# Kernel tuning notes

Measured on AMD Instinct MI355X. Metric: run time of the kernel, lower is better.

## Reference

```python
import jax, jax.numpy as jnp
import numpy as np

N = 100000      # num_nodes
E = 1600000     # num_edges (avg degree 16)
D_IN = 128
D_H = 128
D_OUT = 128


def _init_linear(key, out_dim, in_dim):
    # Kaiming-uniform-like init, bound = 1/sqrt(fan_in)
    bound = 1.0 / np.sqrt(in_dim)
    return jax.random.uniform(key, (out_dim, in_dim), jnp.float32, -bound, bound)


def setup_inputs() -> dict:
    key = jax.random.key(0)
    ks = jax.random.split(key, 12)
    x = jax.random.normal(ks[0], (N, D_IN), jnp.float32)
    edge_index = jax.random.randint(ks[1], (2, E), 0, N, jnp.int32)
    dims = [(D_H, D_IN), (D_H, D_H), (D_OUT, D_H)]
    inp = {"x": x, "edge_index": edge_index}
    for i, (do, di) in enumerate(dims):
        inp[f"Wl{i}"] = _init_linear(ks[2 + 3 * i], do, di)      # lin_l: applied to aggregated neighbors
        inp[f"bl{i}"] = jnp.zeros((do,), jnp.float32)
        inp[f"Wr{i}"] = _init_linear(ks[3 + 3 * i], do, di)      # lin_r: applied to root (self) features
    return inp


def _sage_conv(x, src, dst, Wl, bl, Wr):
    # mean aggregation of source-node features at destination nodes
    msg = x[src]                                                   # [E, d]
    agg = jax.ops.segment_sum(msg, dst, num_segments=N)            # [N, d]
    deg = jax.ops.segment_sum(jnp.ones((src.shape[0],), x.dtype), dst, num_segments=N)
    mean = agg / jnp.maximum(deg, 1.0)[:, None]
    return mean @ Wl.T + bl + x @ Wr.T


def reference(x, edge_index, Wl0, bl0, Wr0, Wl1, bl1, Wr1, Wl2, bl2, Wr2):
    src, dst = edge_index[0], edge_index[1]
    # dropout is identity in eval mode
    h = jax.nn.relu(_sage_conv(x, src, dst, Wl0, bl0, Wr0))
    h = jax.nn.relu(_sage_conv(h, src, dst, Wl1, bl1, Wr1))
    return _sage_conv(h, src, dst, Wl2, bl2, Wr2)
```

## Files before the change

kernel.cpp:

```cpp
#include <hip/hip_runtime.h>
#include <hip/hip_bf16.h>

typedef __attribute__((ext_vector_type(8))) short bf16x8;
typedef __attribute__((ext_vector_type(4))) float f32x4;

#define D 128
#define P2CAP 8192


__global__ __launch_bounds__(256) void k_setup(
    const float* __restrict__ x,
    const float* __restrict__ w0, const float* __restrict__ w1,
    const float* __restrict__ w2, const float* __restrict__ w3,
    const float* __restrict__ w4, const float* __restrict__ w5,
    __hip_bfloat16* __restrict__ xb, __hip_bfloat16* __restrict__ wb,
    int* __restrict__ bhist, int xpair)
{
    int t = blockIdx.x * 256 + threadIdx.x;
    if (t < 512) bhist[t] = 0;
    if (t < xpair) {
        float2 f = ((const float2*)x)[t];
        ((__hip_bfloat162*)xb)[t] = __float22bfloat162_rn(f);
    }
    if (t < 6 * 8192) {
        int wsel = t >> 13, wi = t & 8191;
        const float* wp = w0;
        if (wsel == 1) wp = w1;
        else if (wsel == 2) wp = w2;
        else if (wsel == 3) wp = w3;
        else if (wsel == 4) wp = w4;
        else if (wsel == 5) wp = w5;
        float2 f = ((const float2*)wp)[wi];
        ((__hip_bfloat162*)wb)[t] = __float22bfloat162_rn(f);
    }
}


__global__ __launch_bounds__(256) void k_p0(const int* __restrict__ dst,
                                            int* __restrict__ bhist, int e, int n, int epb) {
    __shared__ int lh[512];
    for (int i = threadIdx.x; i < 512; i += 256) lh[i] = 0;
    __syncthreads();
    int lo = blockIdx.x * epb;
    int hi = lo + epb; if (hi > e) hi = e;
    for (int i = lo + threadIdx.x; i < hi; i += 256) {
        int d = dst[i]; d = ((unsigned)d < (unsigned)n) ? d : 0;
        atomicAdd(&lh[d >> 8], 1);
    }
    __syncthreads();
    for (int i = threadIdx.x; i < 512; i += 256)
        if (lh[i]) atomicAdd(&bhist[i], lh[i]);
}

__global__ void k_bscan(const int* __restrict__ bhist, int* __restrict__ bbase,
                        int* __restrict__ bcursor, int nb) {
    __shared__ int lds[512];
    int t = threadIdx.x;
    int v = (t < nb) ? bhist[t] : 0;
    lds[t] = v;
    __syncthreads();
    for (int off = 1; off < 512; off <<= 1) {
        int x = (t >= off) ? lds[t - off] : 0;
        __syncthreads();
        lds[t] += x;
        __syncthreads();
    }
    if (t < nb) { int b = lds[t] - v; bbase[t] = b; bcursor[t] = b; }
    if (t == nb) bbase[t] = lds[nb - 1];
}

__global__ __launch_bounds__(256) void k_p1(const int* __restrict__ src,
                                            const int* __restrict__ dst,
                                            int* __restrict__ bcursor,
                                            int* __restrict__ tmp, int e, int n, int epb) {
    __shared__ int lh[512], gb[512];
    for (int i = threadIdx.x; i < 512; i += 256) lh[i] = 0;
    __syncthreads();
    int lo = blockIdx.x * epb;
    int hi = lo + epb; if (hi > e) hi = e;
    for (int i = lo + threadIdx.x; i < hi; i += 256) {
        int d = dst[i]; d = ((unsigned)d < (unsigned)n) ? d : 0;
        atomicAdd(&lh[d >> 8], 1);
    }
    __syncthreads();
    for (int i = threadIdx.x; i < 512; i += 256) {
        int c = lh[i];
        gb[i] = c ? atomicAdd(&bcursor[i], c) : 0;
    }
    __syncthreads();
    for (int i = threadIdx.x; i < 512; i += 256) lh[i] = 0;
    __syncthreads();
    for (int i = lo + threadIdx.x; i < hi; i += 256) {
        int d = dst[i]; d = ((unsigned)d < (unsigned)n) ? d : 0;
        int s = src[i]; s = ((unsigned)s < (unsigned)n) ? s : 0;
        int b = d >> 8;
        int p = gb[b] + atomicAdd(&lh[b], 1);
        tmp[p] = s | ((d & 255) << 17);
    }
}

__global__ __launch_bounds__(256) void k_p2(const int* __restrict__ tmp,
                                            const int* __restrict__ bbase,
                                            int* __restrict__ deg, int* __restrict__ offs,
                                            int* __restrict__ csr, int n) {
    __shared__ int hist[256], loc[256], cur[256];
    __shared__ int out[P2CAP];
    int b = blockIdx.x, t = threadIdx.x;
    int base = bbase[b];
    int cnt = bbase[b + 1] - base;
    int nodes = n - b * 256; if (nodes > 256) nodes = 256;
    hist[t] = 0;
    __syncthreads();
    for (int i = t; i < cnt; i += 256)
        atomicAdd(&hist[(tmp[base + i] >> 17) & 255], 1);
    __syncthreads();
    int v = hist[t];
    loc[t] = v;
    __syncthreads();
    for (int off = 1; off < 256; off <<= 1) {
        int x = (t >= off) ? loc[t - off] : 0;
        __syncthreads();
        loc[t] += x;
        __syncthreads();
    }
    int myloc = loc[t] - v;
    cur[t] = myloc;
    if (t < nodes) { deg[b * 256 + t] = v; offs[b * 256 + t] = base + myloc; }
    __syncthreads();
    if (cnt <= P2CAP) {
        for (int i = t; i < cnt; i += 256) {
            int e = tmp[base + i];
            int p = atomicAdd(&cur[(e >> 17) & 255], 1);
            out[p] = e & 0x1FFFF;
        }
        __syncthreads();
        for (int i = t; i < cnt; i += 256) csr[base + i] = out[i];
    } else {
        for (int i = t; i < cnt; i += 256) {
            int e = tmp[base + i];
            int p = atomicAdd(&cur[(e >> 17) & 255], 1);
            csr[base + p] = e & 0x1FFFF;
        }
    }
}


__device__ __forceinline__ void acc_int4(float* acc, int4 d) {
    acc[0] += __uint_as_float((unsigned)d.x << 16);
    acc[1] += __uint_as_float((unsigned)d.x & 0xffff0000u);
    acc[2] += __uint_as_float((unsigned)d.y << 16);
    acc[3] += __uint_as_float((unsigned)d.y & 0xffff0000u);
    acc[4] += __uint_as_float((unsigned)d.z << 16);
    acc[5] += __uint_as_float((unsigned)d.z & 0xffff0000u);
    acc[6] += __uint_as_float((unsigned)d.w << 16);
    acc[7] += __uint_as_float((unsigned)d.w & 0xffff0000u);
}

__global__ __launch_bounds__(256) void k_agg(
    const __hip_bfloat16* __restrict__ h,
    const int* __restrict__ csr,
    const int* __restrict__ offs,
    const int* __restrict__ deg,
    __hip_bfloat16* __restrict__ mean,
    int n)
{
    int node = blockIdx.x * 4 + (threadIdx.x >> 6);
    int lane = threadIdx.x & 63;
    if (node >= n) return;
    int grp = lane >> 4;
    int sub = lane & 15;
    int start = offs[node];
    int cnt = deg[node];

    float acc[8];
    #pragma unroll
    for (int k = 0; k < 8; ++k) acc[k] = 0.f;

    const char* hb = (const char*)h;
    int i = 0;
    int bulk = cnt & ~15;

    for (; i < bulk; i += 16) {
        int4 d[4];
        #pragma unroll
        for (int u = 0; u < 4; ++u) {
            int s = csr[start + i + u * 4 + grp];
            s = ((unsigned)s < (unsigned)n) ? s : 0;
            d[u] = *(const int4*)(hb + (size_t)s * 256 + sub * 16);
        }
        #pragma unroll
        for (int u = 0; u < 4; ++u) acc_int4(acc, d[u]);
    }

    if (i < cnt) {
        int4 d[4];
        #pragma unroll
        for (int u = 0; u < 4; ++u) {
            int e = i + u * 4 + grp;
            int ec = (e < cnt) ? e : (cnt - 1);
            int s = csr[start + ec];
            s = ((unsigned)s < (unsigned)n) ? s : 0;
            d[u] = *(const int4*)(hb + (size_t)s * 256 + sub * 16);
            if (e >= cnt) { d[u].x = 0; d[u].y = 0; d[u].z = 0; d[u].w = 0; }
        }
        #pragma unroll
        for (int u = 0; u < 4; ++u) acc_int4(acc, d[u]);
    }

    #pragma unroll
    for (int k = 0; k < 8; ++k) {
        acc[k] += __shfl_xor(acc[k], 16);
        acc[k] += __shfl_xor(acc[k], 32);
    }

    if (grp == 0) {
        float inv = 1.0f / fmaxf((float)cnt, 1.0f);
        union { int4 i4; __hip_bfloat162 h2[4]; } u;
        #pragma unroll
        for (int k = 0; k < 4; ++k)
            u.h2[k] = __float22bfloat162_rn(make_float2(acc[2 * k] * inv, acc[2 * k + 1] * inv));
        *(int4*)((char*)mean + (size_t)node * 256 + sub * 16) = u.i4;
    }
}


__global__ __launch_bounds__(256) void k_gemm(
    const __hip_bfloat16* __restrict__ A0,
    const __hip_bfloat16* __restrict__ A1,
    const __hip_bfloat16* __restrict__ Wb,
    const float* __restrict__ bias,
    float* __restrict__ outF,
    __hip_bfloat16* __restrict__ outB,
    int n, int do_relu)
{
    __shared__ __hip_bfloat16 lW[2 * 128 * 128];

    for (int g = threadIdx.x; g < 4096; g += 256) {
        int half = g >> 11;
        int rem  = g & 2047;
        int row  = rem >> 4;
        int c    = rem & 15;
        bf16x8 v = *(const bf16x8*)(Wb + half * 16384 + row * 128 + c * 8);
        *(bf16x8*)(lW + half * 16384 + row * 128 + ((c ^ (row & 7)) * 8)) = v;
    }
    __syncthreads();

    int w = threadIdx.x >> 6;
    int lane = threadIdx.x & 63;
    int m = lane & 15;
    int q = lane >> 4;
    int base = blockIdx.x * 256 + w * 64;

    f32x4 acc[4][8];
    #pragma unroll
    for (int r = 0; r < 4; ++r)
        #pragma unroll
        for (int i = 0; i < 8; ++i) acc[r][i] = (f32x4){0.f, 0.f, 0.f, 0.f};

    const __hip_bfloat16* Aps[2] = {A0, A1};

    #pragma unroll
    for (int half = 0; half < 2; ++half) {
        const __hip_bfloat16* A = Aps[half];
        #pragma unroll
        for (int kk = 0; kk < 4; ++kk) {
            bf16x8 af[4];
            #pragma unroll
            for (int r = 0; r < 4; ++r) {
                int arow = base + r * 16 + m;
                if (arow > n - 1) arow = n - 1;
                af[r] = *(const bf16x8*)(A + (size_t)arow * D + kk * 32 + q * 8);
            }
            #pragma unroll
            for (int nt = 0; nt < 8; ++nt) {
                int row = nt * 16 + m;
                int c = (kk * 4 + q) ^ (m & 7);
                bf16x8 bf = *(const bf16x8*)(lW + half * 16384 + row * 128 + c * 8);
                #pragma unroll
                for (int r = 0; r < 4; ++r)
                    acc[r][nt] = __builtin_amdgcn_mfma_f32_16x16x32_bf16(af[r], bf, acc[r][nt], 0, 0, 0);
            }
        }
    }

    #pragma unroll
    for (int r = 0; r < 4; ++r) {
        #pragma unroll
        for (int nt = 0; nt < 8; ++nt) {
            int col = nt * 16 + m;
            float b = bias[col];
            #pragma unroll
            for (int rr = 0; rr < 4; ++rr) {
                int row = base + r * 16 + q * 4 + rr;
                if (row < n) {
                    float v = acc[r][nt][rr] + b;
                    if (do_relu) v = fmaxf(v, 0.f);
                    if (outF) outF[(size_t)row * D + col] = v;
                    else      outB[(size_t)row * D + col] = __float2bfloat16(v);
                }
            }
        }
    }
}


extern "C" void kernel_launch(void* const* d_in, const int* in_sizes, int n_in,
                              void* d_out, int out_size, void* d_ws, size_t ws_size,
                              hipStream_t stream) {
    const float* x   = (const float*)d_in[0];
    const int*   ei  = (const int*)d_in[1];
    const float* Wl0 = (const float*)d_in[2];
    const float* bl0 = (const float*)d_in[3];
    const float* Wr0 = (const float*)d_in[4];
    const float* Wl1 = (const float*)d_in[5];
    const float* bl1 = (const float*)d_in[6];
    const float* Wr1 = (const float*)d_in[7];
    const float* Wl2 = (const float*)d_in[8];
    const float* bl2 = (const float*)d_in[9];
    const float* Wr2 = (const float*)d_in[10];

    const int n = in_sizes[0] / D;
    const int e = in_sizes[1] / 2;
    const int* src = ei;
    const int* dst = ei + e;
    const int nb = (n + 255) >> 8;

    uintptr_t p = ((uintptr_t)d_ws + 255) & ~(uintptr_t)255;
    auto carve = [&](size_t bytes) {
        uintptr_t r = p;
        p = (p + bytes + 255) & ~(uintptr_t)255;
        return (void*)r;
    };
    int* deg     = (int*)carve((size_t)n * 4);
    int* offs    = (int*)carve((size_t)n * 4);
    int* bhist   = (int*)carve(512 * 4);
    int* bbase   = (int*)carve(513 * 4);
    int* bcursor = (int*)carve(512 * 4);
    int* csr     = (int*)carve((size_t)e * 4);
    __hip_bfloat16* mean = (__hip_bfloat16*)carve((size_t)n * D * 2);
    __hip_bfloat16* F1   = (__hip_bfloat16*)carve((size_t)n * D * 2);
    __hip_bfloat16* Wb   = (__hip_bfloat16*)carve((size_t)6 * D * D * 2);
    (void)ws_size; (void)n_in; (void)out_size;

    __hip_bfloat16* h0 = (__hip_bfloat16*)d_out;
    int* tmp = (int*)((char*)d_out + (size_t)n * D * 2);

    const int xpair = n * D / 2;

    k_setup<<<(xpair + 255) / 256, 256, 0, stream>>>(
        x, Wl0, Wr0, Wl1, Wr1, Wl2, Wr2, F1, Wb, bhist, xpair);

    const int epb0 = (e + 511) / 512;
    k_p0<<<512, 256, 0, stream>>>(dst, bhist, e, n, epb0);
    k_bscan<<<1, 512, 0, stream>>>(bhist, bbase, bcursor, nb);
    const int epb1 = 8192;
    k_p1<<<(e + epb1 - 1) / epb1, 256, 0, stream>>>(src, dst, bcursor, tmp, e, n, epb1);
    k_p2<<<nb, 256, 0, stream>>>(tmp, bbase, deg, offs, csr, n);

    const int ag = (n + 3) / 4;
    const int gg = (n + 255) / 256;

    __hip_bfloat16* Wb0 = Wb + 0 * 2 * D * D;
    __hip_bfloat16* Wb1 = Wb + 1 * 2 * D * D;
    __hip_bfloat16* Wb2 = Wb + 2 * 2 * D * D;

    k_agg<<<ag, 256, 0, stream>>>(F1, csr, offs, deg, mean, n);
    k_gemm<<<gg, 256, 0, stream>>>(mean, F1, Wb0, bl0, nullptr, h0, n, 1);
    k_agg<<<ag, 256, 0, stream>>>(h0, csr, offs, deg, mean, n);
    k_gemm<<<gg, 256, 0, stream>>>(mean, h0, Wb1, bl1, nullptr, F1, n, 1);
    k_agg<<<ag, 256, 0, stream>>>(F1, csr, offs, deg, mean, n);
    k_gemm<<<gg, 256, 0, stream>>>(mean, F1, Wb2, bl2, (float*)d_out, nullptr, n, 0);
}
```

Measured before the change: 437.9 us.

## Fuse histogram into setup, pack aggregation math, widen GEMM blocks

Merges the destination-bucket histogram pass into the setup conversion kernel and zeroes the histogram with a memset, which removes one launch. The aggregation kernel now accumulates in packed float2 vectors, drops the index bounds clamp and uses 32-bit address arithmetic to cut ALU work. The GEMM runs 512 threads per block, each wave holding 32 rows instead of 64, which lowers register pressure and adds waves. The scatter pass also uses smaller edge chunks. Removing the clamp means an out-of-range index would now read out of bounds.

```diff
diff --git a/kernel.cpp b/kernel.cpp
--- a/kernel.cpp
+++ b/kernel.cpp
@@ -3,6 +3,7 @@
 
 typedef __attribute__((ext_vector_type(8))) short bf16x8;
 typedef __attribute__((ext_vector_type(4))) float f32x4;
+typedef __attribute__((ext_vector_type(2))) float f32x2;
 
 #define D 128
 #define P2CAP 8192
@@ -14,10 +15,10 @@
     const float* __restrict__ w2, const float* __restrict__ w3,
     const float* __restrict__ w4, const float* __restrict__ w5,
     __hip_bfloat16* __restrict__ xb, __hip_bfloat16* __restrict__ wb,
-    int* __restrict__ bhist, int xpair)
+    int* __restrict__ bhist, const int* __restrict__ dst,
+    int xpair, int e, int n, int epb)
 {
     int t = blockIdx.x * 256 + threadIdx.x;
-    if (t < 512) bhist[t] = 0;
     if (t < xpair) {
         float2 f = ((const float2*)x)[t];
         ((__hip_bfloat162*)xb)[t] = __float22bfloat162_rn(f);
@@ -33,24 +34,22 @@
         float2 f = ((const float2*)wp)[wi];
         ((__hip_bfloat162*)wb)[t] = __float22bfloat162_rn(f);
     }
-}
-
-
-__global__ __launch_bounds__(256) void k_p0(const int* __restrict__ dst,
-                                            int* __restrict__ bhist, int e, int n, int epb) {
-    __shared__ int lh[512];
-    for (int i = threadIdx.x; i < 512; i += 256) lh[i] = 0;
-    __syncthreads();
-    int lo = blockIdx.x * epb;
-    int hi = lo + epb; if (hi > e) hi = e;
-    for (int i = lo + threadIdx.x; i < hi; i += 256) {
-        int d = dst[i]; d = ((unsigned)d < (unsigned)n) ? d : 0;
-        atomicAdd(&lh[d >> 8], 1);
-    }
-    __syncthreads();
-    for (int i = threadIdx.x; i < 512; i += 256)
-        if (lh[i]) atomicAdd(&bhist[i], lh[i]);
-}
+    if (blockIdx.x < 512) {
+        __shared__ int lh[512];
+        for (int i = threadIdx.x; i < 512; i += 256) lh[i] = 0;
+        __syncthreads();
+        int lo = blockIdx.x * epb;
+        int hi = lo + epb; if (hi > e) hi = e;
+        for (int i = lo + threadIdx.x; i < hi; i += 256) {
+            int d = dst[i]; d = ((unsigned)d < (unsigned)n) ? d : 0;
+            atomicAdd(&lh[d >> 8], 1);
+        }
+        __syncthreads();
+        for (int i = threadIdx.x; i < 512; i += 256)
+            if (lh[i]) atomicAdd(&bhist[i], lh[i]);
+    }
+}
+
 
 __global__ void k_bscan(const int* __restrict__ bhist, int* __restrict__ bbase,
                         int* __restrict__ bcursor, int nb) {
@@ -145,15 +144,18 @@
 }
 
 
-__device__ __forceinline__ void acc_int4(float* acc, int4 d) {
-    acc[0] += __uint_as_float((unsigned)d.x << 16);
-    acc[1] += __uint_as_float((unsigned)d.x & 0xffff0000u);
-    acc[2] += __uint_as_float((unsigned)d.y << 16);
-    acc[3] += __uint_as_float((unsigned)d.y & 0xffff0000u);
-    acc[4] += __uint_as_float((unsigned)d.z << 16);
-    acc[5] += __uint_as_float((unsigned)d.z & 0xffff0000u);
-    acc[6] += __uint_as_float((unsigned)d.w << 16);
-    acc[7] += __uint_as_float((unsigned)d.w & 0xffff0000u);
+__device__ __forceinline__ void acc_u32(f32x2& a, unsigned p) {
+    f32x2 c;
+    c.x = __uint_as_float(p << 16);
+    c.y = __uint_as_float(p & 0xffff0000u);
+    a += c;
+}
+
+__device__ __forceinline__ void acc_i4(f32x2* acc, int4 d) {
+    acc_u32(acc[0], (unsigned)d.x);
+    acc_u32(acc[1], (unsigned)d.y);
+    acc_u32(acc[2], (unsigned)d.z);
+    acc_u32(acc[3], (unsigned)d.w);
 }
 
 __global__ __launch_bounds__(256) void k_agg(
@@ -172,24 +174,27 @@
     int start = offs[node];
     int cnt = deg[node];
 
-    float acc[8];
-    #pragma unroll
-    for (int k = 0; k < 8; ++k) acc[k] = 0.f;
+    f32x2 acc[4];
+    #pragma unroll
+    for (int k = 0; k < 4; ++k) acc[k] = (f32x2){0.f, 0.f};
 
     const char* hb = (const char*)h;
+    unsigned suboff = (unsigned)sub * 16u;
+    const int* cp = csr + start + grp;
+
     int i = 0;
     int bulk = cnt & ~15;
 
     for (; i < bulk; i += 16) {
+        int s[4];
+        #pragma unroll
+        for (int u = 0; u < 4; ++u) s[u] = cp[i + u * 4];
         int4 d[4];
         #pragma unroll
-        for (int u = 0; u < 4; ++u) {
-            int s = csr[start + i + u * 4 + grp];
-            s = ((unsigned)s < (unsigned)n) ? s : 0;
-            d[u] = *(const int4*)(hb + (size_t)s * 256 + sub * 16);
-        }
-        #pragma unroll
-        for (int u = 0; u < 4; ++u) acc_int4(acc, d[u]);
+        for (int u = 0; u < 4; ++u)
+            d[u] = *(const int4*)(hb + (((unsigned)s[u] << 8) | suboff));
+        #pragma unroll
+        for (int u = 0; u < 4; ++u) acc_i4(acc, d[u]);
     }
 
     if (i < cnt) {
@@ -199,18 +204,19 @@
             int e = i + u * 4 + grp;
             int ec = (e < cnt) ? e : (cnt - 1);
             int s = csr[start + ec];
-            s = ((unsigned)s < (unsigned)n) ? s : 0;
-            d[u] = *(const int4*)(hb + (size_t)s * 256 + sub * 16);
-            if (e >= cnt) { d[u].x = 0; d[u].y = 0; d[u].z = 0; d[u].w = 0; }
-        }
-        #pragma unroll
-        for (int u = 0; u < 4; ++u) acc_int4(acc, d[u]);
-    }
-
-    #pragma unroll
-    for (int k = 0; k < 8; ++k) {
-        acc[k] += __shfl_xor(acc[k], 16);
-        acc[k] += __shfl_xor(acc[k], 32);
+            d[u] = *(const int4*)(hb + (((unsigned)s << 8) | suboff));
+            if (e >= cnt) d[u] = make_int4(0, 0, 0, 0);
+        }
+        #pragma unroll
+        for (int u = 0; u < 4; ++u) acc_i4(acc, d[u]);
+    }
+
+    #pragma unroll
+    for (int k = 0; k < 4; ++k) {
+        acc[k].x += __shfl_xor(acc[k].x, 16);
+        acc[k].y += __shfl_xor(acc[k].y, 16);
+        acc[k].x += __shfl_xor(acc[k].x, 32);
+        acc[k].y += __shfl_xor(acc[k].y, 32);
     }
 
     if (grp == 0) {
@@ -218,13 +224,13 @@
         union { int4 i4; __hip_bfloat162 h2[4]; } u;
         #pragma unroll
         for (int k = 0; k < 4; ++k)
-            u.h2[k] = __float22bfloat162_rn(make_float2(acc[2 * k] * inv, acc[2 * k + 1] * inv));
-        *(int4*)((char*)mean + (size_t)node * 256 + sub * 16) = u.i4;
-    }
-}
-
-
-__global__ __launch_bounds__(256) void k_gemm(
+            u.h2[k] = __float22bfloat162_rn(make_float2(acc[k].x * inv, acc[k].y * inv));
+        *(int4*)((char*)mean + (size_t)node * 256 + suboff) = u.i4;
+    }
+}
+
+
+__global__ __launch_bounds__(512) void k_gemm(
     const __hip_bfloat16* __restrict__ A0,
     const __hip_bfloat16* __restrict__ A1,
     const __hip_bfloat16* __restrict__ Wb,
@@ -235,7 +241,7 @@
 {
     __shared__ __hip_bfloat16 lW[2 * 128 * 128];
 
-    for (int g = threadIdx.x; g < 4096; g += 256) {
+    for (int g = threadIdx.x; g < 4096; g += 512) {
         int half = g >> 11;
         int rem  = g & 2047;
         int row  = rem >> 4;
@@ -249,11 +255,11 @@
     int lane = threadIdx.x & 63;
     int m = lane & 15;
     int q = lane >> 4;
-    int base = blockIdx.x * 256 + w * 64;
-
-    f32x4 acc[4][8];
-    #pragma unroll
-    for (int r = 0; r < 4; ++r)
+    int base = blockIdx.x * 256 + w * 32;
+
+    f32x4 acc[2][8];
+    #pragma unroll
+    for (int r = 0; r < 2; ++r)
         #pragma unroll
         for (int i = 0; i < 8; ++i) acc[r][i] = (f32x4){0.f, 0.f, 0.f, 0.f};
 
@@ -264,9 +270,9 @@
         const __hip_bfloat16* A = Aps[half];
         #pragma unroll
         for (int kk = 0; kk < 4; ++kk) {
-            bf16x8 af[4];
+            bf16x8 af[2];
             #pragma unroll
-            for (int r = 0; r < 4; ++r) {
+            for (int r = 0; r < 2; ++r) {
                 int arow = base + r * 16 + m;
                 if (arow > n - 1) arow = n - 1;
                 af[r] = *(const bf16x8*)(A + (size_t)arow * D + kk * 32 + q * 8);
@@ -277,14 +283,14 @@
                 int c = (kk * 4 + q) ^ (m & 7);
                 bf16x8 bf = *(const bf16x8*)(lW + half * 16384 + row * 128 + c * 8);
                 #pragma unroll
-                for (int r = 0; r < 4; ++r)
+                for (int r = 0; r < 2; ++r)
                     acc[r][nt] = __builtin_amdgcn_mfma_f32_16x16x32_bf16(af[r], bf, acc[r][nt], 0, 0, 0);
             }
         }
     }
 
     #pragma unroll
-    for (int r = 0; r < 4; ++r) {
+    for (int r = 0; r < 2; ++r) {
         #pragma unroll
         for (int nt = 0; nt < 8; ++nt) {
             int col = nt * 16 + m;
@@ -347,13 +353,13 @@
 
     const int xpair = n * D / 2;
 
+    hipMemsetAsync(bhist, 0, 512 * 4, stream);
+    const int epb0 = (e + 511) / 512;
     k_setup<<<(xpair + 255) / 256, 256, 0, stream>>>(
-        x, Wl0, Wr0, Wl1, Wr1, Wl2, Wr2, F1, Wb, bhist, xpair);
-
-    const int epb0 = (e + 511) / 512;
-    k_p0<<<512, 256, 0, stream>>>(dst, bhist, e, n, epb0);
+        x, Wl0, Wr0, Wl1, Wr1, Wl2, Wr2, F1, Wb, bhist, dst, xpair, e, n, epb0);
+
     k_bscan<<<1, 512, 0, stream>>>(bhist, bbase, bcursor, nb);
-    const int epb1 = 8192;
+    const int epb1 = 2048;
     k_p1<<<(e + epb1 - 1) / epb1, 256, 0, stream>>>(src, dst, bcursor, tmp, e, n, epb1);
     k_p2<<<nb, 256, 0, stream>>>(tmp, bbase, deg, offs, csr, n);
 
@@ -365,9 +371,9 @@
     __hip_bfloat16* Wb2 = Wb + 2 * 2 * D * D;
 
     k_agg<<<ag, 256, 0, stream>>>(F1, csr, offs, deg, mean, n);
-    k_gemm<<<gg, 256, 0, stream>>>(mean, F1, Wb0, bl0, nullptr, h0, n, 1);
+    k_gemm<<<gg, 512, 0, stream>>>(mean, F1, Wb0, bl0, nullptr, h0, n, 1);
     k_agg<<<ag, 256, 0, stream>>>(h0, csr, offs, deg, mean, n);
-    k_gemm<<<gg, 256, 0, stream>>>(mean, h0, Wb1, bl1, nullptr, F1, n, 1);
+    k_gemm<<<gg, 512, 0, stream>>>(mean, h0, Wb1, bl1, nullptr, F1, n, 1);
     k_agg<<<ag, 256, 0, stream>>>(F1, csr, offs, deg, mean, n);
-    k_gemm<<<gg, 256, 0, stream>>>(mean, F1, Wb2, bl2, (float*)d_out, nullptr, n, 0);
-}
+    k_gemm<<<gg, 512, 0, stream>>>(mean, F1, Wb2, bl2, (float*)d_out, nullptr, n, 0);
+}
```

Measured after the change: 414.0 us. 1.06x faster.
